# Kernel tuning notes

Measured on AMD Instinct MI355X. Metric: run time of the kernel, lower is better.

## Reference

```python
import jax, jax.numpy as jnp
import numpy as np

N, F, U, H = 4096, 512, 64, 8
EDGE_PROB = 0.01
NEG_MASK = -10e9  # matches keras-gat masking constant
LRELU_SLOPE = 0.2


def setup_inputs() -> dict:
    key = jax.random.key(0)
    kX, kA, kI, kW, kS, kN, kB = jax.random.split(key, 7)
    X = jax.random.normal(kX, (1, N, F), dtype=jnp.float32)
    # sparse binary adjacency with self loops (layer expects preprocessed self-loops)
    A = (jax.random.uniform(kA, (N, N)) < EDGE_PROB).astype(jnp.float32)
    A = jnp.maximum(A, jnp.eye(N, dtype=jnp.float32))
    out_indices = jax.random.randint(kI, (1, 128), 0, N).astype(jnp.int64)
    scale_w = 1.0 / np.sqrt(F)
    scale_a = 1.0 / np.sqrt(U)
    W = jax.random.normal(kW, (H, F, U), dtype=jnp.float32) * scale_w
    a_self = jax.random.normal(kS, (H, U), dtype=jnp.float32) * scale_a
    a_neigh = jax.random.normal(kN, (H, U), dtype=jnp.float32) * scale_a
    bias = jax.random.normal(kB, (H, U), dtype=jnp.float32) * 0.1
    return {"X": X, "out_indices": out_indices, "A": A, "W": W,
            "a_self": a_self, "a_neigh": a_neigh, "bias": bias}


def reference(X, out_indices, A, W, a_self, a_neigh, bias):
    x = X[0]  # [N, F] (batch dim of 1)
    # per-head linear transform: [H, N, U]
    h = jnp.einsum('nf,hfu->hnu', x, W)
    # additive attention logits: f_self[i] + f_neigh[j]
    f_self = jnp.einsum('hnu,hu->hn', h, a_self)    # [H, N]
    f_neigh = jnp.einsum('hnu,hu->hn', h, a_neigh)  # [H, N]
    scores = f_self[:, :, None] + f_neigh[:, None, :]  # [H, N, N]
    scores = jax.nn.leaky_relu(scores, negative_slope=LRELU_SLOPE)
    # mask non-edges (standard, non-saliency path): dense += -10e9 * (1 - A)
    scores = scores + NEG_MASK * (1.0 - A)[None, :, :]
    attn = jax.nn.softmax(scores, axis=-1)  # [H, N, N]
    # weighted aggregation + bias
    out = jnp.einsum('hnm,hmu->hnu', attn, h) + bias[:, None, :]  # [H, N, U]
    # concat heads: [N, H*U], then activation (relu)
    out = jnp.transpose(out, (1, 0, 2)).reshape(N, H * U)
    out = jax.nn.relu(out)
    return out[None, :, :]  # [1, N, H*U]; final_layer=False -> all nodes
```

## Files before the change

### kernel.cpp

```cpp
#include <hip/hip_runtime.h>
#include <hip/hip_bf16.h>

#define N_NODES 4096
#define F_DIM   512
#define U_DIM   64
#define H_HEADS 8
#define C_DIM   512
#define LRELU_S 0.2f
#define MAXE    128
#define GEMM_BLOCKS 512
#define SCAN_BLOCKS 512
#define ROWS_PER_WAVE 2

typedef __attribute__((ext_vector_type(8))) short bf16x8;
typedef __attribute__((ext_vector_type(4))) float f32x4;

__device__ inline unsigned short f2bf(float f) {
  union { float f; unsigned u; } v; v.f = f;
  unsigned r = v.u + 0x7FFFu + ((v.u >> 16) & 1u);
  return (unsigned short)(r >> 16);
}
__device__ inline float bf2f(unsigned short b) {
  union { unsigned u; float f; } v; v.u = ((unsigned)b) << 16;
  return v.f;
}

__global__ __launch_bounds__(256) void front_kernel(
    const float* __restrict__ X, const float* __restrict__ W,
    const float* __restrict__ A, const float* __restrict__ a_self,
    const float* __restrict__ a_neigh, unsigned short* __restrict__ hb,
    float* __restrict__ fsT, float* __restrict__ fnT, int* __restrict__ deg,
    unsigned short* __restrict__ nbr) {
  __shared__ unsigned short As[64][72];
  __shared__ unsigned short Bs[64][72];

  const int t    = threadIdx.x;
  const int lane = t & 63;
  const int w    = t >> 6;

  if ((int)blockIdx.x < GEMM_BLOCKS) {
    const int mblk = blockIdx.x & 63;
    const int head = blockIdx.x >> 6;
    const int m0   = mblk * 64;
    const float* Wh = W + (size_t)head * F_DIM * U_DIM;

    const int wr = w >> 1, wc = w & 1;
    const int arow = t >> 2;
    const int akc  = (t & 3) * 16;
    const int bu   = t & 63;
    const int bjc  = (t >> 6) * 16;

    f32x4 acc[2][2] = {};

    for (int k0 = 0; k0 < F_DIM; k0 += 64) {
      {
        const float* src = X + (size_t)(m0 + arow) * F_DIM + k0 + akc;
        float4 f0 = ((const float4*)src)[0];
        float4 f1 = ((const float4*)src)[1];
        float4 f2 = ((const float4*)src)[2];
        float4 f3 = ((const float4*)src)[3];
        bf16x8 u0 = {(short)f2bf(f0.x), (short)f2bf(f0.y), (short)f2bf(f0.z),
                     (short)f2bf(f0.w), (short)f2bf(f1.x), (short)f2bf(f1.y),
                     (short)f2bf(f1.z), (short)f2bf(f1.w)};
        bf16x8 u1 = {(short)f2bf(f2.x), (short)f2bf(f2.y), (short)f2bf(f2.z),
                     (short)f2bf(f2.w), (short)f2bf(f3.x), (short)f2bf(f3.y),
                     (short)f2bf(f3.z), (short)f2bf(f3.w)};
        *(bf16x8*)&As[arow][akc]     = u0;
        *(bf16x8*)&As[arow][akc + 8] = u1;
      }
      {
        float bv[16];
#pragma unroll
        for (int j = 0; j < 16; ++j)
          bv[j] = Wh[(size_t)(k0 + bjc + j) * U_DIM + bu];
        bf16x8 w0 = {(short)f2bf(bv[0]), (short)f2bf(bv[1]), (short)f2bf(bv[2]),
                     (short)f2bf(bv[3]), (short)f2bf(bv[4]), (short)f2bf(bv[5]),
                     (short)f2bf(bv[6]), (short)f2bf(bv[7])};
        bf16x8 w1 = {(short)f2bf(bv[8]),  (short)f2bf(bv[9]),
                     (short)f2bf(bv[10]), (short)f2bf(bv[11]),
                     (short)f2bf(bv[12]), (short)f2bf(bv[13]),
                     (short)f2bf(bv[14]), (short)f2bf(bv[15])};
        *(bf16x8*)&Bs[bu][bjc]     = w0;
        *(bf16x8*)&Bs[bu][bjc + 8] = w1;
      }
      __syncthreads();

      const int r  = lane & 15;
      const int ko = (lane >> 4) * 8;
#pragma unroll
      for (int kk = 0; kk < 2; ++kk) {
        bf16x8 af0 = *(const bf16x8*)&As[wr * 32 + r][kk * 32 + ko];
        bf16x8 af1 = *(const bf16x8*)&As[wr * 32 + 16 + r][kk * 32 + ko];
        bf16x8 bf0 = *(const bf16x8*)&Bs[wc * 32 + r][kk * 32 + ko];
        bf16x8 bf1 = *(const bf16x8*)&Bs[wc * 32 + 16 + r][kk * 32 + ko];
        acc[0][0] = __builtin_amdgcn_mfma_f32_16x16x32_bf16(af0, bf0, acc[0][0], 0, 0, 0);
        acc[0][1] = __builtin_amdgcn_mfma_f32_16x16x32_bf16(af0, bf1, acc[0][1], 0, 0, 0);
        acc[1][0] = __builtin_amdgcn_mfma_f32_16x16x32_bf16(af1, bf0, acc[1][0], 0, 0, 0);
        acc[1][1] = __builtin_amdgcn_mfma_f32_16x16x32_bf16(af1, bf1, acc[1][1], 0, 0, 0);
      }
      __syncthreads();
    }

#pragma unroll
    for (int mi = 0; mi < 2; ++mi) {
#pragma unroll
      for (int ni = 0; ni < 2; ++ni) {
        const int rb = wr * 32 + mi * 16 + (lane >> 4) * 4;
        const int cl = wc * 32 + ni * 16 + (lane & 15);
#pragma unroll
        for (int reg = 0; reg < 4; ++reg) {
          unsigned short hv = f2bf(acc[mi][ni][reg]);
          hb[(size_t)(m0 + rb + reg) * C_DIM + head * U_DIM + cl] = hv;
          As[rb + reg][cl] = hv;
        }
      }
    }
    __syncthreads();
    if (t < 128) {
      const int r = t & 63;
      const float* avec = (t >= 64) ? a_neigh + head * U_DIM
                                    : a_self + head * U_DIM;
      float s = 0.f;
#pragma unroll
      for (int u = 0; u < 64; ++u) s += bf2f(As[r][u]) * avec[u];
      float* dst = (t >= 64) ? fnT : fsT;
      dst[(size_t)(m0 + r) * H_HEADS + head] = s;
    }
  } else {
    const int sb = (int)blockIdx.x - GEMM_BLOCKS;
#pragma unroll
    for (int rr = 0; rr < ROWS_PER_WAVE; ++rr) {
      const int i = (sb * 4 + w) * ROWS_PER_WAVE + rr;
      const float* Arow = A + (size_t)i * N_NODES;
      float4 buf[16];
#pragma unroll
      for (int q = 0; q < 16; ++q)
        buf[q] = *(const float4*)(Arow + q * 256 + 4 * lane);

      int c = 0;
#pragma unroll
      for (int q = 0; q < 16; ++q) {
        c += (buf[q].x != 0.f) ? 1 : 0;
        c += (buf[q].y != 0.f) ? 1 : 0;
        c += (buf[q].z != 0.f) ? 1 : 0;
        c += (buf[q].w != 0.f) ? 1 : 0;
      }
      int psum = c;
#pragma unroll
      for (int off = 1; off < 64; off <<= 1) {
        int v = __shfl_up(psum, off);
        if (lane >= off) psum += v;
      }
      const int E = __shfl(psum, 63);
      int pos = psum - c;
      unsigned short* nrow = nbr + (size_t)i * MAXE;
#pragma unroll
      for (int q = 0; q < 16; ++q) {
        const int gb = q * 256 + 4 * lane;
        if (buf[q].x != 0.f) { if (pos < MAXE) nrow[pos] = (unsigned short)(gb);     ++pos; }
        if (buf[q].y != 0.f) { if (pos < MAXE) nrow[pos] = (unsigned short)(gb + 1); ++pos; }
        if (buf[q].z != 0.f) { if (pos < MAXE) nrow[pos] = (unsigned short)(gb + 2); ++pos; }
        if (buf[q].w != 0.f) { if (pos < MAXE) nrow[pos] = (unsigned short)(gb + 3); ++pos; }
      }
      if (lane == 63) deg[i] = (E > MAXE) ? MAXE : E;
    }
  }
}

__global__ __launch_bounds__(256) void attn_kernel(
    const unsigned short* __restrict__ hb, const float* __restrict__ fsT,
    const float* __restrict__ fnT, const float* __restrict__ bias,
    const int* __restrict__ deg, const unsigned short* __restrict__ nbr,
    float* __restrict__ out) {
  __shared__ int   eidx[4][MAXE];
  __shared__ float p[4][MAXE][9];

  const int t    = threadIdx.x;
  const int lane = t & 63;
  const int w    = t >> 6;
  const int i    = blockIdx.x * 4 + w;
  const int E    = deg[i];

  float fsv[8];
  {
    float4 a = *(const float4*)(fsT + (size_t)i * H_HEADS);
    float4 b = *(const float4*)(fsT + (size_t)i * H_HEADS + 4);
    fsv[0]=a.x; fsv[1]=a.y; fsv[2]=a.z; fsv[3]=a.w;
    fsv[4]=b.x; fsv[5]=b.y; fsv[6]=b.z; fsv[7]=b.w;
  }

  float pmax[8];
#pragma unroll
  for (int h = 0; h < 8; ++h) pmax[h] = -1e30f;
  for (int e = lane; e < E; e += 64) {
    const int j = (int)nbr[(size_t)i * MAXE + e];
    eidx[w][e] = j;
    float4 a = *(const float4*)(fnT + (size_t)j * H_HEADS);
    float4 b = *(const float4*)(fnT + (size_t)j * H_HEADS + 4);
    float fnv[8] = {a.x, a.y, a.z, a.w, b.x, b.y, b.z, b.w};
#pragma unroll
    for (int h = 0; h < 8; ++h) {
      float sc = fsv[h] + fnv[h];
      sc = (sc > 0.f) ? sc : LRELU_S * sc;
      p[w][e][h] = sc;
      pmax[h] = fmaxf(pmax[h], sc);
    }
  }
#pragma unroll
  for (int h = 0; h < 8; ++h)
#pragma unroll
    for (int off = 32; off > 0; off >>= 1)
      pmax[h] = fmaxf(pmax[h], __shfl_xor(pmax[h], off));

  float psum[8] = {};
  for (int e = lane; e < E; e += 64) {
#pragma unroll
    for (int h = 0; h < 8; ++h) {
      float ex = __expf(p[w][e][h] - pmax[h]);
      p[w][e][h] = ex;
      psum[h] += ex;
    }
  }
#pragma unroll
  for (int h = 0; h < 8; ++h)
#pragma unroll
    for (int off = 32; off > 0; off >>= 1) psum[h] += __shfl_xor(psum[h], off);

  __syncthreads();

  const int cbase = 8 * lane;
  const int hl = lane >> 3;
  float acc[8] = {};
  for (int e = 0; e < E; ++e) {
    const int j = eidx[w][e];
    uint4 v = *(const uint4*)(hb + (size_t)j * C_DIM + cbase);
    const float pe = p[w][e][hl];
    acc[0] += pe * bf2f((unsigned short)(v.x & 0xFFFFu));
    acc[1] += pe * bf2f((unsigned short)(v.x >> 16));
    acc[2] += pe * bf2f((unsigned short)(v.y & 0xFFFFu));
    acc[3] += pe * bf2f((unsigned short)(v.y >> 16));
    acc[4] += pe * bf2f((unsigned short)(v.z & 0xFFFFu));
    acc[5] += pe * bf2f((unsigned short)(v.z >> 16));
    acc[6] += pe * bf2f((unsigned short)(v.w & 0xFFFFu));
    acc[7] += pe * bf2f((unsigned short)(v.w >> 16));
  }
  float sum = psum[0];
#pragma unroll
  for (int h = 1; h < 8; ++h)
    if (hl == h) sum = psum[h];
  const float inv = 1.0f / sum;

  float4 b0 = *(const float4*)(bias + cbase);
  float4 b1 = *(const float4*)(bias + cbase + 4);
  float4 o0, o1;
  o0.x = fmaxf(acc[0] * inv + b0.x, 0.f);
  o0.y = fmaxf(acc[1] * inv + b0.y, 0.f);
  o0.z = fmaxf(acc[2] * inv + b0.z, 0.f);
  o0.w = fmaxf(acc[3] * inv + b0.w, 0.f);
  o1.x = fmaxf(acc[4] * inv + b1.x, 0.f);
  o1.y = fmaxf(acc[5] * inv + b1.y, 0.f);
  o1.z = fmaxf(acc[6] * inv + b1.z, 0.f);
  o1.w = fmaxf(acc[7] * inv + b1.w, 0.f);
  *(float4*)(out + (size_t)i * C_DIM + cbase)     = o0;
  *(float4*)(out + (size_t)i * C_DIM + cbase + 4) = o1;
}

extern "C" void kernel_launch(void* const* d_in, const int* in_sizes, int n_in,
                              void* d_out, int out_size, void* d_ws,
                              size_t ws_size, hipStream_t stream) {
  const float* X       = (const float*)d_in[0];
  const float* A       = (const float*)d_in[2];
  const float* W       = (const float*)d_in[3];
  const float* a_self  = (const float*)d_in[4];
  const float* a_neigh = (const float*)d_in[5];
  const float* bias    = (const float*)d_in[6];
  float* out = (float*)d_out;

  unsigned short* hb = (unsigned short*)d_ws;
  float* fsT = (float*)(hb + (size_t)N_NODES * C_DIM);
  float* fnT = fsT + (size_t)H_HEADS * N_NODES;
  int* deg   = (int*)(fnT + (size_t)H_HEADS * N_NODES);
  unsigned short* nbr = (unsigned short*)(deg + N_NODES);

  front_kernel<<<GEMM_BLOCKS + SCAN_BLOCKS, 256, 0, stream>>>(
      X, W, A, a_self, a_neigh, hb, fsT, fnT, deg, nbr);

  attn_kernel<<<N_NODES / 4, 256, 0, stream>>>(hb, fsT, fnT, bias, deg, nbr,
                                               out);
}
```

Baseline: 43.86 us.

## Compact adjacency rows with ballot masks, one block per row, scan blocks first

The adjacency scan now gives each of the 4096 rows its own 256-thread block. Each wave handles a quarter of the row and builds per-position ballot masks, so positions come from popcounts rather than a per-lane serial loop after a shuffle scan. The scan blocks are placed before the GEMM blocks in the grid, which spreads the 64MB adjacency read across many more blocks and so more memory parallelism. The cost is many more small blocks, plus a shared-memory sync per row.

```diff
diff --git a/kernel.cpp b/kernel.cpp
--- a/kernel.cpp
+++ b/kernel.cpp
@@ -8,9 +8,6 @@
 #define C_DIM   512
 #define LRELU_S 0.2f
 #define MAXE    128
-#define GEMM_BLOCKS 512
-#define SCAN_BLOCKS 512
-#define ROWS_PER_WAVE 2
 
 typedef __attribute__((ext_vector_type(8))) short bf16x8;
 typedef __attribute__((ext_vector_type(4))) float f32x4;
@@ -33,14 +30,60 @@
     unsigned short* __restrict__ nbr) {
   __shared__ unsigned short As[64][72];
   __shared__ unsigned short Bs[64][72];
+  __shared__ int wsum[4];
 
   const int t    = threadIdx.x;
   const int lane = t & 63;
   const int w    = t >> 6;
 
-  if ((int)blockIdx.x < GEMM_BLOCKS) {
-    const int mblk = blockIdx.x & 63;
-    const int head = blockIdx.x >> 6;
+  if ((int)blockIdx.x < N_NODES) {
+    const int i = (int)blockIdx.x;
+    const float* Aq = A + (size_t)i * N_NODES + w * 1024;
+    float4 v0 = *(const float4*)(Aq +   0 + 4 * lane);
+    float4 v1 = *(const float4*)(Aq + 256 + 4 * lane);
+    float4 v2 = *(const float4*)(Aq + 512 + 4 * lane);
+    float4 v3 = *(const float4*)(Aq + 768 + 4 * lane);
+
+    unsigned long long mk[16];
+    mk[ 0] = __ballot(v0.x != 0.f); mk[ 1] = __ballot(v0.y != 0.f);
+    mk[ 2] = __ballot(v0.z != 0.f); mk[ 3] = __ballot(v0.w != 0.f);
+    mk[ 4] = __ballot(v1.x != 0.f); mk[ 5] = __ballot(v1.y != 0.f);
+    mk[ 6] = __ballot(v1.z != 0.f); mk[ 7] = __ballot(v1.w != 0.f);
+    mk[ 8] = __ballot(v2.x != 0.f); mk[ 9] = __ballot(v2.y != 0.f);
+    mk[10] = __ballot(v2.z != 0.f); mk[11] = __ballot(v2.w != 0.f);
+    mk[12] = __ballot(v3.x != 0.f); mk[13] = __ballot(v3.y != 0.f);
+    mk[14] = __ballot(v3.z != 0.f); mk[15] = __ballot(v3.w != 0.f);
+
+    int cnt = 0;
+#pragma unroll
+    for (int q = 0; q < 16; ++q) cnt += __popcll(mk[q]);
+    if (lane == 0) wsum[w] = cnt;
+    __syncthreads();
+
+    int base = 0;
+#pragma unroll
+    for (int k = 0; k < 4; ++k)
+      if (k < w) base += wsum[k];
+    const int total = wsum[0] + wsum[1] + wsum[2] + wsum[3];
+
+    const unsigned long long lt  = (1ULL << lane) - 1ULL;
+    const unsigned long long bit = 1ULL << lane;
+    unsigned short* nrow = nbr + (size_t)i * MAXE;
+#pragma unroll
+    for (int q = 0; q < 16; ++q) {
+      if (mk[q] & bit) {
+        const int pos = base + (int)__popcll(mk[q] & lt);
+        if (pos < MAXE)
+          nrow[pos] =
+              (unsigned short)(w * 1024 + (q >> 2) * 256 + 4 * lane + (q & 3));
+      }
+      base += (int)__popcll(mk[q]);
+    }
+    if (t == 0) deg[i] = (total > MAXE) ? MAXE : total;
+  } else {
+    const int g    = (int)blockIdx.x - N_NODES;
+    const int mblk = g & 63;
+    const int head = g >> 6;
     const int m0   = mblk * 64;
     const float* Wh = W + (size_t)head * F_DIM * U_DIM;
 
@@ -126,44 +169,6 @@
       float* dst = (t >= 64) ? fnT : fsT;
       dst[(size_t)(m0 + r) * H_HEADS + head] = s;
     }
-  } else {
-    const int sb = (int)blockIdx.x - GEMM_BLOCKS;
-#pragma unroll
-    for (int rr = 0; rr < ROWS_PER_WAVE; ++rr) {
-      const int i = (sb * 4 + w) * ROWS_PER_WAVE + rr;
-      const float* Arow = A + (size_t)i * N_NODES;
-      float4 buf[16];
-#pragma unroll
-      for (int q = 0; q < 16; ++q)
-        buf[q] = *(const float4*)(Arow + q * 256 + 4 * lane);
-
-      int c = 0;
-#pragma unroll
-      for (int q = 0; q < 16; ++q) {
-        c += (buf[q].x != 0.f) ? 1 : 0;
-        c += (buf[q].y != 0.f) ? 1 : 0;
-        c += (buf[q].z != 0.f) ? 1 : 0;
-        c += (buf[q].w != 0.f) ? 1 : 0;
-      }
-      int psum = c;
-#pragma unroll
-      for (int off = 1; off < 64; off <<= 1) {
-        int v = __shfl_up(psum, off);
-        if (lane >= off) psum += v;
-      }
-      const int E = __shfl(psum, 63);
-      int pos = psum - c;
-      unsigned short* nrow = nbr + (size_t)i * MAXE;
-#pragma unroll
-      for (int q = 0; q < 16; ++q) {
-        const int gb = q * 256 + 4 * lane;
-        if (buf[q].x != 0.f) { if (pos < MAXE) nrow[pos] = (unsigned short)(gb);     ++pos; }
-        if (buf[q].y != 0.f) { if (pos < MAXE) nrow[pos] = (unsigned short)(gb + 1); ++pos; }
-        if (buf[q].z != 0.f) { if (pos < MAXE) nrow[pos] = (unsigned short)(gb + 2); ++pos; }
-        if (buf[q].w != 0.f) { if (pos < MAXE) nrow[pos] = (unsigned short)(gb + 3); ++pos; }
-      }
-      if (lane == 63) deg[i] = (E > MAXE) ? MAXE : E;
-    }
   }
 }
 
@@ -282,7 +287,7 @@
   int* deg   = (int*)(fnT + (size_t)H_HEADS * N_NODES);
   unsigned short* nbr = (unsigned short*)(deg + N_NODES);
 
-  front_kernel<<<GEMM_BLOCKS + SCAN_BLOCKS, 256, 0, stream>>>(
+  front_kernel<<<N_NODES + 512, 256, 0, stream>>>(
       X, W, A, a_self, a_neigh, hb, fsT, fnT, deg, nbr);
 
   attn_kernel<<<N_NODES / 4, 256, 0, stream>>>(hb, fsT, fnT, bias, deg, nbr,
```

Result: slower. 45.33 us (+3.3%).

## Rewrite adjacency scan as one row per wave with ballot compaction

Applied to the files above, without the earlier changes.

The adjacency-scan part of the front kernel now has each wave handle one row instead of two, and the number of scan blocks doubles so more rows are processed in parallel. The shuffle-based prefix sum is replaced by per-element wave ballots and popcount compaction, and the next 1024-column chunk is loaded while the current one is processed. This aims to raise memory-level parallelism while streaming the large dense adjacency matrix and to shorten the serial compaction path. In exchange it issues more ballot and popcount instructions, and neighbor indices come out in a different order, which can slightly change floating-point summation order.

```diff
diff --git a/kernel.cpp b/kernel.cpp
--- a/kernel.cpp
+++ b/kernel.cpp
@@ -9,8 +9,7 @@
 #define LRELU_S 0.2f
 #define MAXE    128
 #define GEMM_BLOCKS 512
-#define SCAN_BLOCKS 512
-#define ROWS_PER_WAVE 2
+#define SCAN_BLOCKS 1024
 
 typedef __attribute__((ext_vector_type(8))) short bf16x8;
 typedef __attribute__((ext_vector_type(4))) float f32x4;
@@ -128,42 +127,52 @@
     }
   } else {
     const int sb = (int)blockIdx.x - GEMM_BLOCKS;
-#pragma unroll
-    for (int rr = 0; rr < ROWS_PER_WAVE; ++rr) {
-      const int i = (sb * 4 + w) * ROWS_PER_WAVE + rr;
-      const float* Arow = A + (size_t)i * N_NODES;
-      float4 buf[16];
-#pragma unroll
-      for (int q = 0; q < 16; ++q)
-        buf[q] = *(const float4*)(Arow + q * 256 + 4 * lane);
-
-      int c = 0;
-#pragma unroll
-      for (int q = 0; q < 16; ++q) {
-        c += (buf[q].x != 0.f) ? 1 : 0;
-        c += (buf[q].y != 0.f) ? 1 : 0;
-        c += (buf[q].z != 0.f) ? 1 : 0;
-        c += (buf[q].w != 0.f) ? 1 : 0;
-      }
-      int psum = c;
-#pragma unroll
-      for (int off = 1; off < 64; off <<= 1) {
-        int v = __shfl_up(psum, off);
-        if (lane >= off) psum += v;
-      }
-      const int E = __shfl(psum, 63);
-      int pos = psum - c;
-      unsigned short* nrow = nbr + (size_t)i * MAXE;
-#pragma unroll
-      for (int q = 0; q < 16; ++q) {
-        const int gb = q * 256 + 4 * lane;
-        if (buf[q].x != 0.f) { if (pos < MAXE) nrow[pos] = (unsigned short)(gb);     ++pos; }
-        if (buf[q].y != 0.f) { if (pos < MAXE) nrow[pos] = (unsigned short)(gb + 1); ++pos; }
-        if (buf[q].z != 0.f) { if (pos < MAXE) nrow[pos] = (unsigned short)(gb + 2); ++pos; }
-        if (buf[q].w != 0.f) { if (pos < MAXE) nrow[pos] = (unsigned short)(gb + 3); ++pos; }
-      }
-      if (lane == 63) deg[i] = (E > MAXE) ? MAXE : E;
-    }
+    const int i  = sb * 4 + w;
+    const float* Arow = A + (size_t)i * N_NODES;
+    unsigned short* nrow = nbr + (size_t)i * MAXE;
+
+    const unsigned long long lt  = (lane == 63) ? 0x7FFFFFFFFFFFFFFFULL
+                                                : ((1ULL << lane) - 1ULL);
+    const unsigned long long bit = 1ULL << lane;
+
+    float4 c0 = *(const float4*)(Arow + lane * 16 + 0);
+    float4 c1 = *(const float4*)(Arow + lane * 16 + 4);
+    float4 c2 = *(const float4*)(Arow + lane * 16 + 8);
+    float4 c3 = *(const float4*)(Arow + lane * 16 + 12);
+
+    int base = 0;
+#pragma unroll
+    for (int q = 0; q < 4; ++q) {
+      float4 n0, n1, n2, n3;
+      if (q < 3) {
+        const float* nx = Arow + (q + 1) * 1024 + lane * 16;
+        n0 = *(const float4*)(nx + 0);
+        n1 = *(const float4*)(nx + 4);
+        n2 = *(const float4*)(nx + 8);
+        n3 = *(const float4*)(nx + 12);
+      }
+      unsigned long long mk[16];
+      mk[ 0] = __ballot(c0.x != 0.f); mk[ 1] = __ballot(c0.y != 0.f);
+      mk[ 2] = __ballot(c0.z != 0.f); mk[ 3] = __ballot(c0.w != 0.f);
+      mk[ 4] = __ballot(c1.x != 0.f); mk[ 5] = __ballot(c1.y != 0.f);
+      mk[ 6] = __ballot(c1.z != 0.f); mk[ 7] = __ballot(c1.w != 0.f);
+      mk[ 8] = __ballot(c2.x != 0.f); mk[ 9] = __ballot(c2.y != 0.f);
+      mk[10] = __ballot(c2.z != 0.f); mk[11] = __ballot(c2.w != 0.f);
+      mk[12] = __ballot(c3.x != 0.f); mk[13] = __ballot(c3.y != 0.f);
+      mk[14] = __ballot(c3.z != 0.f); mk[15] = __ballot(c3.w != 0.f);
+
+      const int ebase = q * 1024 + lane * 16;
+#pragma unroll
+      for (int j = 0; j < 16; ++j) {
+        if (mk[j] & bit) {
+          const int pos = base + (int)__popcll(mk[j] & lt);
+          if (pos < MAXE) nrow[pos] = (unsigned short)(ebase + j);
+        }
+        base += (int)__popcll(mk[j]);
+      }
+      c0 = n0; c1 = n1; c2 = n2; c3 = n3;
+    }
+    if (lane == 0) deg[i] = (base > MAXE) ? MAXE : base;
   }
 }
 
```

Result: faster. 41.66 us (-5.0%).
